# Performance work log

Hardware: AMD Instinct MI355X
Metric: run time of the kernel (lower is better)

## Reference

```python
import jax, jax.numpy as jnp
import numpy as np

# --- low precision float format: exp=5, man=2, subnormals, nearest-even ---
EXP, MAN = 5, 2
BIAS = 2 ** (EXP - 1) - 1          # 15
EMIN = 1 - BIAS                     # -14 (min normal exponent; clamping here gives subnormals)
MAXV = (2.0 - 2.0 ** (-MAN)) * 2.0 ** BIAS


def _q(x):
    """Round x to nearest FP(exp=5, man=2) value (subnormals, clipped at max)."""
    ax = jnp.abs(x)
    e = jnp.floor(jnp.log2(jnp.where(ax > 0, ax, 1.0)))
    e = jnp.maximum(e, EMIN)
    scale = jnp.exp2(e - MAN)
    q = jnp.round(x / scale) * scale   # jnp.round = half-to-even
    q = jnp.clip(q, -MAXV, MAXV)
    return jnp.where(ax > 0, q, x).astype(x.dtype)


# Quantizer: forward quantize, straight-through (quantized) backward
@jax.custom_vjp
def fq(x):
    return _q(x)

def _fq_fwd(x):
    return _q(x), None

def _fq_bwd(_, g):
    return (_q(g),)

fq.defvjp(_fq_fwd, _fq_bwd)


def conv_valid(x, w):
    return jax.lax.conv_general_dilated(
        x, w, window_strides=(1, 1), padding='VALID',
        dimension_numbers=('NCHW', 'OIHW', 'NCHW'))


def qconv(x, w):
    # QConv2d: input_quant, weight_quant, conv, output_quant
    return fq(conv_valid(fq(x), fq(w)))


def qlinear(x, W, b):
    # QLinear: input_quant, weight_quant (weights + bias), matmul, output_quant
    return fq(fq(x) @ fq(W).T + fq(b))


def batchnorm(x, gamma, beta, eps=1e-5):
    # training-mode BatchNorm2d over (N,H,W) per channel
    m = x.mean(axis=(0, 2, 3), keepdims=True)
    v = x.var(axis=(0, 2, 3), keepdims=True)
    return (x - m) * jax.lax.rsqrt(v + eps) * gamma[None, :, None, None] + beta[None, :, None, None]


def maxpool2(x):
    return jax.lax.reduce_window(x, -jnp.inf, jax.lax.max,
                                 (1, 1, 2, 2), (1, 1, 2, 2), 'VALID')


def setup_inputs() -> dict:
    key = jax.random.key(0)
    ks = jax.random.split(key, 12)
    B = 8192
    inp = {
        'x':   jax.random.normal(ks[0], (B, 1, 32, 32), jnp.float32),
        'w1':  jax.random.normal(ks[1], (6, 1, 5, 5), jnp.float32) * 0.2,
        'g1':  jnp.ones((6,), jnp.float32),
        'be1': jnp.zeros((6,), jnp.float32),
        'w2':  jax.random.normal(ks[2], (16, 6, 5, 5), jnp.float32) * 0.1,
        'g2':  jnp.ones((16,), jnp.float32),
        'be2': jnp.zeros((16,), jnp.float32),
        'fw1': jax.random.normal(ks[3], (120, 400), jnp.float32) * 0.05,
        'fb1': jnp.zeros((120,), jnp.float32),
        'fw2': jax.random.normal(ks[4], (84, 120), jnp.float32) * 0.09,
        'fb2': jnp.zeros((84,), jnp.float32),
        'fw3': jax.random.normal(ks[5], (10, 84), jnp.float32) * 0.1,
        'fb3': jnp.zeros((10,), jnp.float32),
    }
    return inp


def reference(x, w1, g1, be1, w2, g2, be2, fw1, fb1, fw2, fb2, fw3, fb3):
    x = fq(x)                                   # act_error_quant
    x = qconv(x, w1)                            # conv1 (no bias)
    x = batchnorm(x, g1, be1)                   # bn1
    x = fq(x)                                   # act_error_quant
    x = maxpool2(jax.nn.relu(x))                # relu + 2x2 maxpool -> [B,6,14,14]
    x = qconv(x, w2)                            # conv2 -> [B,16,10,10]
    x = batchnorm(x, g2, be2)                   # bn2
    x = fq(x)
    x = maxpool2(jax.nn.relu(x))                # -> [B,16,5,5]
    x = x.reshape(x.shape[0], -1)               # [B,400]
    x = jax.nn.relu(qlinear(x, fw1, fb1))       # fc1
    x = jax.nn.relu(qlinear(x, fw2, fb2))       # fc2
    x = qlinear(x, fw3, fb3)                    # fc3 -> [B,10]
    return x
```

## Files before the change

### kernel.cpp

```cpp
#include <hip/hip_runtime.h>
#include <hip/hip_bf16.h>


#define BATCH 8192

typedef double d4 __attribute__((ext_vector_type(4)));

__device__ __forceinline__ double fq_d(double x) {
    long long b = __double_as_longlong(x);
    long long ab = b & 0x7fffffffffffffffLL;
    if (ab == 0) return x;
    double q;
    if (ab >= 0x3F10000000000000LL) {
        long long r = b + 0x0001FFFFFFFFFFFFLL + ((b >> 50) & 1LL);
        r &= 0xFFFC000000000000LL;
        q = __longlong_as_double(r);
        q = fmin(fmax(q, -57344.0), 57344.0);
    } else {
        q = rint(x * 65536.0) * 1.52587890625e-05;
    }
    return q;
}

__device__ __forceinline__ float fq_f(float x) {
    int b = __float_as_int(x);
    int ab = b & 0x7fffffff;
    if (ab == 0) return x;
    float q;
    if (ab >= 0x38800000) {
        int r = b + 0x000FFFFF + ((b >> 21) & 1);
        r &= 0xFFE00000;
        q = __int_as_float(r);
        q = fminf(fmaxf(q, -57344.0f), 57344.0f);
    } else {
        q = rintf(x * 65536.0f) * 1.52587890625e-05f;
    }
    return q;
}

__device__ __forceinline__ unsigned short bfbits(double q) {
    __hip_bfloat16 h = __float2bfloat16((float)q);
    return *(unsigned short*)&h;
}

__device__ __forceinline__ float bfval(unsigned short u) {
    return __bfloat162float(*(__hip_bfloat16*)&u);
}

__global__ void kprep(const float* __restrict__ w1, const float* __restrict__ w2,
                      const float* __restrict__ fb1, const float* __restrict__ fb2,
                      const float* __restrict__ fb3, const float* __restrict__ fw1,
                      const float* __restrict__ fw2, const float* __restrict__ fw3,
                      float* __restrict__ qw1, float* __restrict__ qw2t,
                      float* __restrict__ qfb1, float* __restrict__ qfb2,
                      float* __restrict__ qfb3, float* __restrict__ Wt1,
                      float* __restrict__ Wt2, float* __restrict__ Wt3) {
    int i = blockIdx.x * 256 + threadIdx.x;
    if (i < 150) { qw1[i] = fq_f(w1[i]); return; }
    i -= 150;
    if (i < 2432) { int k = i >> 4, co = i & 15;
        qw2t[i] = (k < 150) ? fq_f(w2[co * 150 + k]) : 0.0f; return; }
    i -= 2432;
    if (i < 120) { qfb1[i] = fq_f(fb1[i]); return; }
    i -= 120;
    if (i < 84) { qfb2[i] = fq_f(fb2[i]); return; }
    i -= 84;
    if (i < 10) { qfb3[i] = fq_f(fb3[i]); return; }
    i -= 10;
    if (i < 51200) { int k = i / 128, o = i % 128;
        Wt1[i] = (o < 120) ? fq_f(fw1[o * 400 + k]) : 0.0f; return; }
    i -= 51200;
    if (i < 15360) { int k = i / 128, o = i % 128;
        Wt2[i] = (o < 84) ? fq_f(fw2[o * 120 + k]) : 0.0f; return; }
    i -= 15360;
    if (i < 1344) { int k = i / 16, o = i % 16;
        Wt3[i] = (o < 10) ? fq_f(fw3[o * 84 + k]) : 0.0f; return; }
}
#define PREP_TOTAL (150 + 2432 + 120 + 84 + 10 + 51200 + 15360 + 1344)

__global__ __launch_bounds__(512) void kconv1(const float* __restrict__ x,
        const float* __restrict__ qw, const float* __restrict__ g1,
        unsigned short* __restrict__ praw, int nimg_total,
        double* __restrict__ st1) {
    __shared__ float sxf[3 * 1056];
    __shared__ double swd[152];
    __shared__ float sg1[6];
    __shared__ double sred[6][2];
    int t = threadIdx.x;
    int b0 = blockIdx.x * 3;
    int nimg = nimg_total - b0; if (nimg > 3) nimg = 3;
    for (int i = t; i < nimg * 1024; i += 512) {
        int img = i >> 10, idx = i & 1023;
        sxf[img * 1056 + (idx >> 5) * 33 + (idx & 31)] =
            fq_f(x[(size_t)(b0 + img) * 1024 + idx]);
    }
    if (t < 150) swd[t] = (double)qw[t];
    if (t >= 160 && t < 166) sg1[t - 160] = g1[t - 160];
    if (t >= 192 && t < 204) ((double*)sred)[t - 192] = 0.0;
    __syncthreads();
    int ntask = nimg * 168;
    for (int task = t; task < ntask; task += 512) {
        int img = task / 168; int rr = task % 168;
        int co = rr / 28; int rem = rr % 28;
        int ph = rem >> 1;
        int half = rem & 1;
        int i0 = 2 * ph;
        int j0 = half * 14;
        const double* wp = &swd[co * 25];
        double a0[14], a1[14];
        #pragma unroll
        for (int j = 0; j < 14; ++j) { a0[j] = 0.0; a1[j] = 0.0; }
        double wr[5], wq[5];
        #pragma unroll
        for (int u = 0; u < 6; ++u) {
            const float* xr = &sxf[img * 1056 + (i0 + u) * 33 + j0];
            double xv[18];
            #pragma unroll
            for (int k = 0; k < 18; ++k) xv[k] = (double)xr[k];
            if (u < 5) {
                #pragma unroll
                for (int tt = 0; tt < 5; ++tt) wr[tt] = wp[u * 5 + tt];
                #pragma unroll
                for (int j = 0; j < 14; ++j)
                    a0[j] = fma(xv[j], wr[0], fma(xv[j+1], wr[1], fma(xv[j+2], wr[2],
                            fma(xv[j+3], wr[3], fma(xv[j+4], wr[4], a0[j])))));
            }
            if (u >= 1) {
                #pragma unroll
                for (int j = 0; j < 14; ++j)
                    a1[j] = fma(xv[j], wq[0], fma(xv[j+1], wq[1], fma(xv[j+2], wq[2],
                            fma(xv[j+3], wq[3], fma(xv[j+4], wq[4], a1[j])))));
            }
            #pragma unroll
            for (int tt = 0; tt < 5; ++tt) wq[tt] = wr[tt];
        }
        double q0[14], q1[14];
        double s = 0.0, s2 = 0.0;
        #pragma unroll
        for (int j = 0; j < 14; ++j) {
            q0[j] = fq_d(a0[j]); q1[j] = fq_d(a1[j]);
            s += q0[j] + q1[j]; s2 += q0[j] * q0[j] + q1[j] * q1[j];
        }
        bool useMax = (sg1[co] >= 0.0f);
        unsigned short* dst = praw + ((size_t)(b0 + img) * 6 + co) * 196 + ph * 14 + half * 7;
        #pragma unroll
        for (int jp = 0; jp < 7; ++jp) {
            double pmax = fmax(fmax(q0[2*jp], q0[2*jp+1]), fmax(q1[2*jp], q1[2*jp+1]));
            double pmin = fmin(fmin(q0[2*jp], q0[2*jp+1]), fmin(q1[2*jp], q1[2*jp+1]));
            dst[jp] = bfbits(useMax ? pmax : pmin);
        }
        atomicAdd(&sred[co][0], s);
        atomicAdd(&sred[co][1], s2);
    }
    __syncthreads();
    if (t < 12) atomicAdd(&st1[t * 32 + (blockIdx.x & 31)], ((double*)sred)[t]);
}

__global__ __launch_bounds__(512) void kconv2(const unsigned short* __restrict__ praw,
        const double* __restrict__ st1, const float* __restrict__ g1,
        const float* __restrict__ be1, const float* __restrict__ qw2t,
        __hip_bfloat16* __restrict__ c2, double* __restrict__ st2) {
    __shared__ float sxf[9408];
    __shared__ float swf[2432];
    __shared__ int soff[152];
    __shared__ unsigned short sep[8][256];
    __shared__ double sred[16][2];
    __shared__ double sbn1[6][4];
    int t = threadIdx.x;
    int b0 = blockIdx.x * 8;
    {
        const float4* wsrc = (const float4*)qw2t;
        float4* wdst = (float4*)swf;
        for (int i = t; i < 608; i += 512) wdst[i] = wsrc[i];
    }
    if (t < 152)
        soff[t] = (t < 150) ? (t / 25) * 196 + ((t % 25) / 5) * 14 + (t % 5) : 0;
    if (t < 32) ((double*)sred)[t] = 0.0;
    if (t < 6) {
        double s = 0.0, s2 = 0.0;
        for (int b = 0; b < 32; ++b) { s += st1[t * 64 + b]; s2 += st1[t * 64 + 32 + b]; }
        double m = s / 6422528.0;
        double v = s2 / 6422528.0 - m * m;
        sbn1[t][0] = m; sbn1[t][1] = 1.0 / sqrt(v + 1e-5);
        sbn1[t][2] = (double)g1[t]; sbn1[t][3] = (double)be1[t];
    }
    __syncthreads();
    const ushort4* srcp = (const ushort4*)(praw + (size_t)b0 * 1176);
    for (int i = t; i < 2352; i += 512) {
        ushort4 u = srcp[i];
        int ch = ((4 * i) % 1176) / 196;
        double m = sbn1[ch][0], r = sbn1[ch][1];
        double gg = sbn1[ch][2], bb = sbn1[ch][3];
        float* d = &sxf[4 * i];
        double q;
        q = fq_d((((double)bfval(u.x) - m) * r) * gg + bb); d[0] = (float)fmax(q, 0.0);
        q = fq_d((((double)bfval(u.y) - m) * r) * gg + bb); d[1] = (float)fmax(q, 0.0);
        q = fq_d((((double)bfval(u.z) - m) * r) * gg + bb); d[2] = (float)fmax(q, 0.0);
        q = fq_d((((double)bfval(u.w) - m) * r) * gg + bb); d[3] = (float)fmax(q, 0.0);
    }
    __syncthreads();

    int l = t & 63, w = t >> 6;
    int c = l >> 4, r16 = l & 15;

    d4 pz = {0.0, 0.0, 0.0, 0.0};
    d4 prow = __builtin_amdgcn_mfma_f64_16x16x4f64((double)r16, 0.25, pz, 0, 0, 0);
    d4 pcol = __builtin_amdgcn_mfma_f64_16x16x4f64(1.0, 0.25 * (double)r16, pz, 0, 0, 0);
    int rowidx[4], colidx[4];
    #pragma unroll
    for (int j = 0; j < 4; ++j) { rowidx[j] = (int)prow[j]; colidx[j] = (int)pcol[j]; }

    unsigned short* myep = sep[w];
    double ls = 0.0, ls2 = 0.0;
    int co0 = colidx[0];
    for (int tile = w; tile < 50; tile += 8) {
        int pos = tile * 16 + r16;
        int abase = (pos / 100) * 1176 + ((pos % 100) / 10) * 14 + (pos % 10);
        d4 a0 = {0.0, 0.0, 0.0, 0.0}, a1 = {0.0, 0.0, 0.0, 0.0};
        d4 a2 = {0.0, 0.0, 0.0, 0.0}, a3 = {0.0, 0.0, 0.0, 0.0};
        #pragma unroll
        for (int s = 0; s < 10; ++s) {
            int k0 = 4 * s + c;
            int k1 = 4 * (s + 10) + c;
            double x0 = (double)sxf[abase + soff[k0]];
            double w0 = (double)swf[k0 * 16 + r16];
            a0 = __builtin_amdgcn_mfma_f64_16x16x4f64(x0, w0, a0, 0, 0, 0);
            double x1 = (double)sxf[abase + soff[k1]];
            double w1 = (double)swf[k1 * 16 + r16];
            a1 = __builtin_amdgcn_mfma_f64_16x16x4f64(x1, w1, a1, 0, 0, 0);
            if (s < 9) {
                int k2 = 4 * (s + 20) + c;
                int k3 = 4 * (s + 29) + c;
                double x2 = (double)sxf[abase + soff[k2]];
                double w2 = (double)swf[k2 * 16 + r16];
                a2 = __builtin_amdgcn_mfma_f64_16x16x4f64(x2, w2, a2, 0, 0, 0);
                double x3 = (double)sxf[abase + soff[k3]];
                double w3 = (double)swf[k3 * 16 + r16];
                a3 = __builtin_amdgcn_mfma_f64_16x16x4f64(x3, w3, a3, 0, 0, 0);
            }
        }
        #pragma unroll
        for (int j = 0; j < 4; ++j) {
            double q = fq_d((a0[j] + a1[j]) + (a2[j] + a3[j]));
            myep[rowidx[j] * 16 + colidx[j]] = bfbits(q);
            ls += q; ls2 += q * q;
        }
        ushort4 v = *(const ushort4*)&myep[l * 4];
        *(ushort4*)((unsigned short*)c2 + ((size_t)b0 * 100 + tile * 16) * 16 + l * 4) = v;
    }
    atomicAdd(&sred[co0][0], ls);
    atomicAdd(&sred[co0][1], ls2);
    __syncthreads();
    if (t < 32) atomicAdd(&st2[t * 32 + (blockIdx.x & 31)], ((double*)sred)[t]);
}

__global__ __launch_bounds__(256) void kfc1(const __hip_bfloat16* __restrict__ c2,
        const double* __restrict__ st2, const float* __restrict__ g2,
        const float* __restrict__ be2, const float* __restrict__ Wt,
        const float* __restrict__ qb, __hip_bfloat16* __restrict__ outb) {
    constexpr int IN = 400, OUT = 120, OUTP = 128, ROWS = 4, BT = 8;
    __shared__ double sx[BT][IN];
    __shared__ double sbn[16][4];
    int t = threadIdx.x;
    int b0 = blockIdx.x * BT;
    if (t < 16) {
        double s = 0.0, s2 = 0.0;
        for (int b = 0; b < 32; ++b) { s += st2[t * 64 + b]; s2 += st2[t * 64 + 32 + b]; }
        double m = s / (819200.0);
        double v = s2 / (819200.0) - m * m;
        sbn[t][0] = m; sbn[t][1] = 1.0 / sqrt(v + 1e-5);
        sbn[t][2] = (double)g2[t]; sbn[t][3] = (double)be2[t];
    }
    __syncthreads();
    for (int i = t; i < BT * IN; i += 256) {
        int cc = i & 15;
        int rem = (i >> 4) % 25;
        int r = i / 400;
        int ph = rem / 5, pw = rem % 5;
        const __hip_bfloat16* src = c2 + ((size_t)(b0 + r) * 100 + 20 * ph + 2 * pw) * 16 + cc;
        double m = sbn[cc][0], rr = sbn[cc][1], gg = sbn[cc][2], bb = sbn[cc][3];
        float f0 = __bfloat162float(src[0]),   f1 = __bfloat162float(src[16]);
        float f2 = __bfloat162float(src[160]), f3 = __bfloat162float(src[176]);
        bool useMax = (rr * gg) >= 0.0;
        float v = useMax ? fmaxf(fmaxf(f0, f1), fmaxf(f2, f3))
                         : fminf(fminf(f0, f1), fminf(f2, f3));
        double q = fq_d((((double)v - m) * rr) * gg + bb);
        sx[r][cc * 25 + rem] = fmax(q, 0.0);
    }
    __syncthreads();
    int o = t % OUTP;
    int g = t / OUTP;
    double acc[ROWS];
    double bias = (o < OUT) ? (double)qb[o] : 0.0;
    #pragma unroll
    for (int r = 0; r < ROWS; ++r) acc[r] = bias;
    #pragma unroll 4
    for (int k = 0; k < IN; ++k) {
        double w = (double)Wt[k * OUTP + o];
        #pragma unroll
        for (int r = 0; r < ROWS; ++r)
            acc[r] = fma(sx[g * ROWS + r][k], w, acc[r]);
    }
    if (o < OUT) {
        #pragma unroll
        for (int r = 0; r < ROWS; ++r) {
            double q = fq_d(acc[r]);
            if (q < 0.0) q = 0.0;
            outb[(size_t)(b0 + g * ROWS + r) * OUT + o] = __float2bfloat16((float)q);
        }
    }
}

__global__ __launch_bounds__(256) void kfc23(const __hip_bfloat16* __restrict__ a1,
        const float* __restrict__ Wt2, const float* __restrict__ qfb2,
        const float* __restrict__ Wt3, const float* __restrict__ qfb3,
        float* __restrict__ out) {
    __shared__ double sx1[16][120];
    __shared__ double s2[16][84];
    int t = threadIdx.x;
    int b0 = blockIdx.x * 16;
    for (int i = t; i < 16 * 120; i += 256) {
        int r = i / 120, k = i % 120;
        sx1[r][k] = (double)__bfloat162float(a1[(size_t)(b0 + r) * 120 + k]);
    }
    __syncthreads();
    {
        int o = t % 128, g = t / 128;
        double acc[8];
        double bias = (o < 84) ? (double)qfb2[o] : 0.0;
        #pragma unroll
        for (int r = 0; r < 8; ++r) acc[r] = bias;
        #pragma unroll 4
        for (int k = 0; k < 120; ++k) {
            double w = (double)Wt2[k * 128 + o];
            #pragma unroll
            for (int r = 0; r < 8; ++r)
                acc[r] = fma(sx1[g * 8 + r][k], w, acc[r]);
        }
        if (o < 84) {
            #pragma unroll
            for (int r = 0; r < 8; ++r) {
                double q = fq_d(acc[r]);
                s2[g * 8 + r][o] = fmax(q, 0.0);
            }
        }
    }
    __syncthreads();
    {
        int o = t % 16, g = t / 16;
        double acc = (o < 10) ? (double)qfb3[o] : 0.0;
        #pragma unroll 4
        for (int k = 0; k < 84; ++k)
            acc = fma(s2[g][k], (double)Wt3[k * 16 + o], acc);
        if (o < 10)
            out[(size_t)(b0 + g) * 10 + o] = (float)fq_d(acc);
    }
}

extern "C" void kernel_launch(void* const* d_in, const int* in_sizes, int n_in,
                              void* d_out, int out_size, void* d_ws, size_t ws_size,
                              hipStream_t stream) {
    const float* x   = (const float*)d_in[0];
    const float* w1  = (const float*)d_in[1];
    const float* g1  = (const float*)d_in[2];
    const float* be1 = (const float*)d_in[3];
    const float* w2  = (const float*)d_in[4];
    const float* g2  = (const float*)d_in[5];
    const float* be2 = (const float*)d_in[6];
    const float* fw1 = (const float*)d_in[7];
    const float* fb1 = (const float*)d_in[8];
    const float* fw2 = (const float*)d_in[9];
    const float* fb2 = (const float*)d_in[10];
    const float* fw3 = (const float*)d_in[11];
    const float* fb3 = (const float*)d_in[12];

    char* ws = (char*)d_ws;
    double* stats1 = (double*)(ws + 0);
    double* stats2 = (double*)(ws + 3072);
    float* qw1  = (float*)(ws + 12288);
    float* qw2t = (float*)(ws + 13312);
    float* qfb1 = (float*)(ws + 23040);
    float* qfb2 = (float*)(ws + 23552);
    float* qfb3 = (float*)(ws + 24064);
    float* Wt1  = (float*)(ws + 24576);
    float* Wt2  = (float*)(ws + 229376);
    float* Wt3  = (float*)(ws + 290816);
    unsigned short* praw = (unsigned short*)(ws + 303104);
    __hip_bfloat16* c2 = (__hip_bfloat16*)(ws + 19570688);
    __hip_bfloat16* a1 = (__hip_bfloat16*)(ws + 45785088);

    hipMemsetAsync(ws, 0, 11264, stream);

    kprep<<<(PREP_TOTAL + 255) / 256, 256, 0, stream>>>(
        w1, w2, fb1, fb2, fb3, fw1, fw2, fw3,
        qw1, qw2t, qfb1, qfb2, qfb3, Wt1, Wt2, Wt3);

    kconv1<<<(BATCH + 2) / 3, 512, 0, stream>>>(x, qw1, g1, praw, BATCH, stats1);
    kconv2<<<BATCH / 8, 512, 0, stream>>>(praw, stats1, g1, be1, qw2t, c2, stats2);
    kfc1<<<BATCH / 8, 256, 0, stream>>>(c2, stats2, g2, be2, Wt1, qfb1, a1);
    kfc23<<<BATCH / 16, 256, 0, stream>>>(a1, Wt2, qfb2, Wt3, qfb3, (float*)d_out);
}
```

Measured before the change: 373.6 us.

## Fuse fc1, fc2 and fc3 into one kernel and reorder conv1 task mapping

Merges the fc1 kernel and the fc2/fc3 kernel into one kernel that keeps fc1 activations in shared memory. This removes a kernel launch and the global write and read of the intermediate bf16 activations. The fc2/fc3 stages now process 8 rows per block instead of 16, so each weight load is reused across fewer rows. conv1's task index is also reordered so that output channel is the outer dimension.

```diff
diff --git a/kernel.cpp b/kernel.cpp
--- a/kernel.cpp
+++ b/kernel.cpp
@@ -98,10 +98,11 @@
     if (t >= 160 && t < 166) sg1[t - 160] = g1[t - 160];
     if (t >= 192 && t < 204) ((double*)sred)[t - 192] = 0.0;
     __syncthreads();
-    int ntask = nimg * 168;
+    int M = nimg * 28;
+    int ntask = 6 * M;
     for (int task = t; task < ntask; task += 512) {
-        int img = task / 168; int rr = task % 168;
-        int co = rr / 28; int rem = rr % 28;
+        int co = task / M; int r = task % M;
+        int img = r / 28; int rem = r % 28;
         int ph = rem >> 1;
         int half = rem & 1;
         int i0 = 2 * ph;
@@ -254,20 +255,24 @@
     if (t < 32) atomicAdd(&st2[t * 32 + (blockIdx.x & 31)], ((double*)sred)[t]);
 }
 
-__global__ __launch_bounds__(256) void kfc1(const __hip_bfloat16* __restrict__ c2,
+__global__ __launch_bounds__(256) void kfc(const __hip_bfloat16* __restrict__ c2,
         const double* __restrict__ st2, const float* __restrict__ g2,
-        const float* __restrict__ be2, const float* __restrict__ Wt,
-        const float* __restrict__ qb, __hip_bfloat16* __restrict__ outb) {
-    constexpr int IN = 400, OUT = 120, OUTP = 128, ROWS = 4, BT = 8;
+        const float* __restrict__ be2, const float* __restrict__ Wt1,
+        const float* __restrict__ qfb1, const float* __restrict__ Wt2,
+        const float* __restrict__ qfb2, const float* __restrict__ Wt3,
+        const float* __restrict__ qfb3, float* __restrict__ out) {
+    constexpr int IN = 400, BT = 8;
     __shared__ double sx[BT][IN];
+    __shared__ double s1[BT][120];
+    __shared__ double s2[BT][84];
     __shared__ double sbn[16][4];
     int t = threadIdx.x;
     int b0 = blockIdx.x * BT;
     if (t < 16) {
-        double s = 0.0, s2 = 0.0;
-        for (int b = 0; b < 32; ++b) { s += st2[t * 64 + b]; s2 += st2[t * 64 + 32 + b]; }
+        double s = 0.0, ss = 0.0;
+        for (int b = 0; b < 32; ++b) { s += st2[t * 64 + b]; ss += st2[t * 64 + 32 + b]; }
         double m = s / (819200.0);
-        double v = s2 / (819200.0) - m * m;
+        double v = ss / (819200.0) - m * m;
         sbn[t][0] = m; sbn[t][1] = 1.0 / sqrt(v + 1e-5);
         sbn[t][2] = (double)g2[t]; sbn[t][3] = (double)be2[t];
     }
@@ -288,72 +293,60 @@
         sx[r][cc * 25 + rem] = fmax(q, 0.0);
     }
     __syncthreads();
-    int o = t % OUTP;
-    int g = t / OUTP;
-    double acc[ROWS];
-    double bias = (o < OUT) ? (double)qb[o] : 0.0;
-    #pragma unroll
-    for (int r = 0; r < ROWS; ++r) acc[r] = bias;
-    #pragma unroll 4
-    for (int k = 0; k < IN; ++k) {
-        double w = (double)Wt[k * OUTP + o];
-        #pragma unroll
-        for (int r = 0; r < ROWS; ++r)
-            acc[r] = fma(sx[g * ROWS + r][k], w, acc[r]);
-    }
-    if (o < OUT) {
-        #pragma unroll
-        for (int r = 0; r < ROWS; ++r) {
-            double q = fq_d(acc[r]);
-            if (q < 0.0) q = 0.0;
-            outb[(size_t)(b0 + g * ROWS + r) * OUT + o] = __float2bfloat16((float)q);
-        }
-    }
-}
-
-__global__ __launch_bounds__(256) void kfc23(const __hip_bfloat16* __restrict__ a1,
-        const float* __restrict__ Wt2, const float* __restrict__ qfb2,
-        const float* __restrict__ Wt3, const float* __restrict__ qfb3,
-        float* __restrict__ out) {
-    __shared__ double sx1[16][120];
-    __shared__ double s2[16][84];
-    int t = threadIdx.x;
-    int b0 = blockIdx.x * 16;
-    for (int i = t; i < 16 * 120; i += 256) {
-        int r = i / 120, k = i % 120;
-        sx1[r][k] = (double)__bfloat162float(a1[(size_t)(b0 + r) * 120 + k]);
-    }
-    __syncthreads();
     {
         int o = t % 128, g = t / 128;
-        double acc[8];
+        double acc[4];
+        double bias = (o < 120) ? (double)qfb1[o] : 0.0;
+        #pragma unroll
+        for (int r = 0; r < 4; ++r) acc[r] = bias;
+        #pragma unroll 4
+        for (int k = 0; k < IN; ++k) {
+            double w = (double)Wt1[k * 128 + o];
+            #pragma unroll
+            for (int r = 0; r < 4; ++r)
+                acc[r] = fma(sx[g * 4 + r][k], w, acc[r]);
+        }
+        if (o < 120) {
+            #pragma unroll
+            for (int r = 0; r < 4; ++r) {
+                double q = fq_d(acc[r]);
+                s1[g * 4 + r][o] = fmax(q, 0.0);
+            }
+        }
+    }
+    __syncthreads();
+    {
+        int o = t % 128, g = t / 128;
+        double acc[4];
         double bias = (o < 84) ? (double)qfb2[o] : 0.0;
         #pragma unroll
-        for (int r = 0; r < 8; ++r) acc[r] = bias;
+        for (int r = 0; r < 4; ++r) acc[r] = bias;
         #pragma unroll 4
         for (int k = 0; k < 120; ++k) {
             double w = (double)Wt2[k * 128 + o];
             #pragma unroll
-            for (int r = 0; r < 8; ++r)
-                acc[r] = fma(sx1[g * 8 + r][k], w, acc[r]);
+            for (int r = 0; r < 4; ++r)
+                acc[r] = fma(s1[g * 4 + r][k], w, acc[r]);
         }
         if (o < 84) {
             #pragma unroll
-            for (int r = 0; r < 8; ++r) {
+            for (int r = 0; r < 4; ++r) {
                 double q = fq_d(acc[r]);
-                s2[g * 8 + r][o] = fmax(q, 0.0);
+                s2[g * 4 + r][o] = fmax(q, 0.0);
             }
         }
     }
     __syncthreads();
     {
         int o = t % 16, g = t / 16;
-        double acc = (o < 10) ? (double)qfb3[o] : 0.0;
-        #pragma unroll 4
-        for (int k = 0; k < 84; ++k)
-            acc = fma(s2[g][k], (double)Wt3[k * 16 + o], acc);
-        if (o < 10)
-            out[(size_t)(b0 + g) * 10 + o] = (float)fq_d(acc);
+        if (g < BT) {
+            double acc = (o < 10) ? (double)qfb3[o] : 0.0;
+            #pragma unroll 4
+            for (int k = 0; k < 84; ++k)
+                acc = fma(s2[g][k], (double)Wt3[k * 16 + o], acc);
+            if (o < 10)
+                out[(size_t)(b0 + g) * 10 + o] = (float)fq_d(acc);
+        }
     }
 }
 
@@ -387,7 +380,6 @@
     float* Wt3  = (float*)(ws + 290816);
     unsigned short* praw = (unsigned short*)(ws + 303104);
     __hip_bfloat16* c2 = (__hip_bfloat16*)(ws + 19570688);
-    __hip_bfloat16* a1 = (__hip_bfloat16*)(ws + 45785088);
 
     hipMemsetAsync(ws, 0, 11264, stream);
 
@@ -397,6 +389,6 @@
 
     kconv1<<<(BATCH + 2) / 3, 512, 0, stream>>>(x, qw1, g1, praw, BATCH, stats1);
     kconv2<<<BATCH / 8, 512, 0, stream>>>(praw, stats1, g1, be1, qw2t, c2, stats2);
-    kfc1<<<BATCH / 8, 256, 0, stream>>>(c2, stats2, g2, be2, Wt1, qfb1, a1);
-    kfc23<<<BATCH / 16, 256, 0, stream>>>(a1, Wt2, qfb2, Wt3, qfb3, (float*)d_out);
-}
+    kfc<<<BATCH / 8, 256, 0, stream>>>(c2, stats2, g2, be2, Wt1, qfb1,
+                                       Wt2, qfb2, Wt3, qfb3, (float*)d_out);
+}
```

Measured after the change: 370.9 us. About the same (-0.7%).
